# Kernel optimization log

Measured on AMD Instinct MI355X. Metric: run time of the kernel, lower is better.

## Reference

```python
import jax, jax.numpy as jnp
import numpy as np

N, E, DIN, EIN, H, R, G, DEPTH = 50000, 800000, 64, 16, 300, 1024, 256, 5


def setup_inputs() -> dict:
    key = jax.random.key(0)
    ks = jax.random.split(key, 16)
    x = jax.random.normal(ks[0], (N, DIN), jnp.float32)
    edge_attr = jax.random.normal(ks[1], (E, EIN), jnp.float32)
    edge_index = jax.random.randint(ks[2], (2, E), 0, N, dtype=jnp.int32)
    batch = jnp.sort(jax.random.randint(ks[3], (N,), 0, G, dtype=jnp.int32))
    def lin(k, fan_in, shape):
        return jax.random.normal(k, shape, jnp.float32) / np.sqrt(fan_in)
    return {
        "x": x,
        "edge_attr": edge_attr,
        "edge_index": edge_index,
        "batch": batch,
        "W_pn": lin(ks[4], DIN, (DIN, H)),
        "b_pn": jnp.zeros((H,), jnp.float32),
        "W_pe": lin(ks[5], EIN, (EIN, H)),
        "b_pe": jnp.zeros((H,), jnp.float32),
        "W1": lin(ks[6], H, (DEPTH, H, H)),
        "b1": jnp.zeros((DEPTH, H), jnp.float32),
        "W2": lin(ks[7], H, (DEPTH, H, H)),
        "b2": jnp.zeros((DEPTH, H), jnp.float32),
        "W_sp": lin(ks[8], H, (H, R)),
        "b_sp": jnp.zeros((R,), jnp.float32),
        "prelu_a": jnp.float32(0.25),
    }


def reference(x, edge_attr, edge_index, batch, W_pn, b_pn, W_pe, b_pe,
              W1, b1, W2, b2, W_sp, b_sp, prelu_a):
    src = edge_index[0]  # message source (x_j)
    dst = edge_index[1]  # aggregation target
    # input projections
    h = jax.nn.relu(x @ W_pn + b_pn)          # [N, H]
    e = edge_attr @ W_pe + b_pe               # [E, H]
    for i in range(DEPTH):
        # GINEConv: sum_j ReLU(x_j + e_ji), eps = 0
        m = jax.nn.relu(h[src] + e)            # [E, H]
        agg = jax.ops.segment_sum(m, dst, num_segments=N)  # [N, H]
        z = h + agg
        z = jax.nn.relu(z @ W1[i] + b1[i]) @ W2[i] + b2[i]
        h = jax.nn.relu(z) if i < DEPTH - 1 else z
        # dropout is identity in eval mode
    pooled = jax.ops.segment_sum(h, batch, num_segments=G)  # [G, H]
    out = pooled @ W_sp + b_sp                 # [G, R]
    # PReLU with a single learned slope
    return jnp.where(out >= 0, out, prelu_a * out)
```

## Files before the change

kernel.cpp:

```cpp
#include <hip/hip_runtime.h>
#include <hip/hip_bf16.h>

#define N_NODES 50000
#define N_EDGES 800000
#define DIN_    64
#define EIN_    16
#define H_      300
#define R_OUT   1024
#define G_GR    256
#define DEPTH_  5
#define KPAD    320
#define NPAD    50048

typedef unsigned short ushort_t;
typedef __attribute__((ext_vector_type(8))) short bf16x8;
typedef __attribute__((ext_vector_type(4))) float f32x4;

__device__ __forceinline__ ushort_t f2b(float f) {
  unsigned x = __float_as_uint(f);
  unsigned r = (x + 0x7fffu + ((x >> 16) & 1u)) >> 16;
  return (ushort_t)r;
}
__device__ __forceinline__ float b2f(ushort_t u) {
  return __uint_as_float((unsigned)u << 16);
}

__global__ void pack_weights(const float* __restrict__ W1, const float* __restrict__ W2,
                             ushort_t* __restrict__ Bp1, ushort_t* __restrict__ Bp2) {
  int idx = blockIdx.x * 256 + threadIdx.x;
  const int per = DEPTH_ * 40 * KPAD * 8;
  if (idx >= 2 * per) return;
  const float* W = W1;
  ushort_t* Bp = Bp1;
  int t = idx;
  if (t >= per) { t -= per; W = W2; Bp = Bp2; }
  int j  = t & 7;
  int n  = (t >> 3) % KPAD;
  int kg = ((t >> 3) / KPAD) % 40;
  int i  = t / (40 * KPAD * 8);
  int k  = kg * 8 + j;
  float v = (k < H_ && n < H_) ? W[(i * H_ + k) * H_ + n] : 0.f;
  Bp[t] = f2b(v);
}

__global__ void pack_wpe(const float* __restrict__ Wpe, const float* __restrict__ bpe,
                         ushort_t* __restrict__ Bpe) {
  int t = blockIdx.x * 256 + threadIdx.x;
  if (t >= 4 * KPAD * 8) return;
  int j  = t & 7;
  int n  = (t >> 3) % KPAD;
  int kg = (t >> 3) / KPAD;
  int k  = kg * 8 + j;
  float v = 0.f;
  if (n < H_) {
    if (k < EIN_) v = Wpe[k * H_ + n];
    else if (k == EIN_) v = bpe[n];
  }
  Bpe[t] = f2b(v);
}

__global__ void hist_deg(const int* __restrict__ dst, int* __restrict__ deg) {
  int e = blockIdx.x * 256 + threadIdx.x;
  if (e < N_EDGES) atomicAdd(deg + dst[e], 1);
}

__global__ __launch_bounds__(1024) void exscan_kernel(const int* __restrict__ deg,
                                                      int* __restrict__ off) {
  __shared__ int wsum[16];
  __shared__ int carry_s;
  int lane = threadIdx.x & 63;
  int wv = threadIdx.x >> 6;
  if (threadIdx.x == 0) carry_s = 0;
  __syncthreads();
  for (int base = 0; base < N_NODES; base += 1024) {
    int i = base + (int)threadIdx.x;
    int orig = (i < N_NODES) ? deg[i] : 0;
    int v = orig;
#pragma unroll
    for (int s = 1; s < 64; s <<= 1) {
      int u = __shfl_up(v, s);
      if (lane >= s) v += u;
    }
    if (lane == 63) wsum[wv] = v;
    __syncthreads();
    if (wv == 0) {
      int t = (lane < 16) ? wsum[lane] : 0;
#pragma unroll
      for (int s = 1; s < 16; s <<= 1) {
        int u = __shfl_up(t, s);
        if (lane >= s) t += u;
      }
      if (lane < 16) wsum[lane] = t;
    }
    __syncthreads();
    int wbase = (wv > 0) ? wsum[wv - 1] : 0;
    if (i < N_NODES) off[i] = carry_s + wbase + v - orig;
    __syncthreads();
    if (threadIdx.x == 1023) carry_s += wsum[15];
    __syncthreads();
  }
  if (threadIdx.x == 0) off[N_NODES] = carry_s;
}

__global__ void scatter_edges(const int* __restrict__ src, const int* __restrict__ dst,
                              int* __restrict__ cursor, int* __restrict__ csr_src,
                              int* __restrict__ csr_eid) {
  int e = blockIdx.x * 256 + threadIdx.x;
  if (e >= N_EDGES) return;
  int d = dst[e];
  int pos = atomicAdd(cursor + d, 1);
  csr_src[pos] = src[e];
  csr_eid[pos] = e;
}

__global__ void proj_nodes(const float* __restrict__ x, const float* __restrict__ Wpn,
                           const float* __restrict__ bpn, ushort_t* __restrict__ hb) {
  unsigned f = blockIdx.x * 256u + threadIdx.x;
  if (f >= (unsigned)NPAD * KPAD) return;
  unsigned n = f / KPAD, hh = f % KPAD;
  float v = 0.f;
  if (n < N_NODES && hh < H_) {
    float acc = bpn[hh];
    const float* xr = x + n * DIN_;
    const float* wc = Wpn + hh;
#pragma unroll 8
    for (int k = 0; k < DIN_; ++k) acc += xr[k] * wc[k * H_];
    v = fmaxf(acc, 0.f);
  }
  hb[f] = f2b(v);
}

__global__ __launch_bounds__(320) void node_agg_mfma(const ushort_t* __restrict__ hb,
                                                     const float* __restrict__ ea,
                                                     const ushort_t* __restrict__ Bpe,
                                                     const int* __restrict__ csr_src,
                                                     const int* __restrict__ csr_eid,
                                                     const int* __restrict__ off,
                                                     ushort_t* zb) {
  int n = blockIdx.x;
  int tid = threadIdx.x;
  if (n >= N_NODES) {
    zb[(unsigned)n * KPAD + tid] = 0;
    return;
  }
  int lane = tid & 63;
  int w = tid >> 6;
  int lr = lane & 15, lg = lane >> 4;
  int p0 = __builtin_amdgcn_readfirstlane(off[n]);
  int p1 = __builtin_amdgcn_readfirstlane(off[n + 1]);

  bf16x8 bfr[4];
#pragma unroll
  for (int t = 0; t < 4; ++t) {
    int col = w * 64 + t * 16 + lr;
    bfr[t] = *(const bf16x8*)(Bpe + ((unsigned)lg * KPAD + col) * 8);
  }

  float msum0 = 0.f, msum1 = 0.f, msum2 = 0.f, msum3 = 0.f;

  for (int pc = p0; pc < p1; pc += 16) {
    int eid = csr_eid[pc + lr];
    bf16x8 afr = (bf16x8){0, 0, 0, 0, 0, 0, 0, 0};
    if (lg < 2) {
      const float* ar = ea + (size_t)eid * EIN_ + lg * 8;
      f32x4 lo = *(const f32x4*)ar;
      f32x4 hi = *(const f32x4*)(ar + 4);
#pragma unroll
      for (int j = 0; j < 4; ++j) {
        afr[j] = (short)f2b(lo[j]);
        afr[j + 4] = (short)f2b(hi[j]);
      }
    } else if (lg == 2) {
      afr[0] = (short)0x3F80;
    }
    int base = pc + 4 * lg;
    int s0 = csr_src[base + 0];
    int s1 = csr_src[base + 1];
    int s2 = csr_src[base + 2];
    int s3 = csr_src[base + 3];
    bool v0 = (base + 0 < p1), v1 = (base + 1 < p1), v2 = (base + 2 < p1), v3 = (base + 3 < p1);
#pragma unroll
    for (int t = 0; t < 4; ++t) {
      int colb = w * 64 + t * 16 + lr;
      float g0 = b2f(hb[(unsigned)s0 * KPAD + colb]);
      float g1 = b2f(hb[(unsigned)s1 * KPAD + colb]);
      float g2 = b2f(hb[(unsigned)s2 * KPAD + colb]);
      float g3 = b2f(hb[(unsigned)s3 * KPAD + colb]);
      f32x4 e4 = __builtin_amdgcn_mfma_f32_16x16x32_bf16(afr, bfr[t], (f32x4){0.f, 0.f, 0.f, 0.f}, 0, 0, 0);
      float m0 = v0 ? fmaxf(g0 + e4[0], 0.f) : 0.f;
      float m1 = v1 ? fmaxf(g1 + e4[1], 0.f) : 0.f;
      float m2 = v2 ? fmaxf(g2 + e4[2], 0.f) : 0.f;
      float m3 = v3 ? fmaxf(g3 + e4[3], 0.f) : 0.f;
      float add = (m0 + m1) + (m2 + m3);
      if (t == 0) msum0 += add;
      else if (t == 1) msum1 += add;
      else if (t == 2) msum2 += add;
      else msum3 += add;
    }
  }

#pragma unroll
  for (int t = 0; t < 4; ++t) {
    float v = (t == 0) ? msum0 : (t == 1) ? msum1 : (t == 2) ? msum2 : msum3;
    v += __shfl_xor(v, 16);
    v += __shfl_xor(v, 32);
    if (lane < 16) {
      unsigned zi = (unsigned)n * KPAD + w * 64 + t * 16 + lane;
      zb[zi] = f2b(b2f(hb[zi]) + v);
    }
  }
}

template <int RELU_OUT, int OUT_BF16>
__global__ __launch_bounds__(256) void gemm300(const ushort_t* A,
                                               const ushort_t* __restrict__ Bp,
                                               const float* __restrict__ bias,
                                               void* Cout) {
  int lane = threadIdx.x & 63;
  int wid  = threadIdx.x >> 6;
  int lr = lane & 15, lg = lane >> 4;
  int rowblk  = blockIdx.x * 64 + (wid & 1) * 32;
  int colbase = (wid >> 1) * 160;
  f32x4 acc[2][10];
#pragma unroll
  for (int a = 0; a < 2; ++a)
#pragma unroll
    for (int c = 0; c < 10; ++c) acc[a][c] = (f32x4){0.f, 0.f, 0.f, 0.f};

  const ushort_t* Ap = A + (unsigned)(rowblk + lr) * KPAD + lg * 8;
  for (int k0 = 0; k0 < KPAD; k0 += 32) {
    bf16x8 a0 = *(const bf16x8*)(Ap + k0);
    bf16x8 a1 = *(const bf16x8*)(Ap + 16 * KPAD + k0);
    const ushort_t* bb = Bp + ((unsigned)(k0 / 8 + lg) * KPAD + colbase + lr) * 8;
#pragma unroll
    for (int c = 0; c < 10; ++c) {
      bf16x8 b = *(const bf16x8*)(bb + c * 16 * 8);
      acc[0][c] = __builtin_amdgcn_mfma_f32_16x16x32_bf16(a0, b, acc[0][c], 0, 0, 0);
      acc[1][c] = __builtin_amdgcn_mfma_f32_16x16x32_bf16(a1, b, acc[1][c], 0, 0, 0);
    }
  }
  __syncthreads();
#pragma unroll
  for (int rt = 0; rt < 2; ++rt) {
#pragma unroll
    for (int c = 0; c < 10; ++c) {
      int col = colbase + c * 16 + lr;
      float bv = (col < H_) ? bias[col] : 0.f;
#pragma unroll
      for (int r = 0; r < 4; ++r) {
        int row = rowblk + rt * 16 + lg * 4 + r;
        if (row >= N_NODES) continue;
        float v = acc[rt][c][r] + bv;
        if (RELU_OUT) v = fmaxf(v, 0.f);
        if (OUT_BF16) {
          ((ushort_t*)Cout)[(unsigned)row * KPAD + col] = f2b(v);
        } else if (col < H_) {
          ((float*)Cout)[(unsigned)row * H_ + col] = v;
        }
      }
    }
  }
}

__global__ void pool_kernel(const float* __restrict__ h, const int* __restrict__ batch,
                            float* __restrict__ pooled) {
  int g = blockIdx.x;
  int hh = threadIdx.x;
  int lo = 0, hi = N_NODES;
  while (lo < hi) { int mid = (lo + hi) >> 1; if (batch[mid] < g) lo = mid + 1; else hi = mid; }
  int start = lo;
  hi = N_NODES;
  while (lo < hi) { int mid = (lo + hi) >> 1; if (batch[mid] < g + 1) lo = mid + 1; else hi = mid; }
  int end = lo;
  if (hh >= H_) return;
  float s = 0.f;
  for (int n = start; n < end; ++n) s += h[(unsigned)n * H_ + hh];
  pooled[g * H_ + hh] = s;
}

__global__ void final_kernel(const float* __restrict__ pooled, const float* __restrict__ Wsp,
                             const float* __restrict__ bsp, const float* __restrict__ pa,
                             float* __restrict__ out) {
  int f = blockIdx.x * 256 + threadIdx.x;
  if (f >= G_GR * R_OUT) return;
  int g = f >> 10, r = f & 1023;
  float acc = bsp[r];
  const float* pr = pooled + g * H_;
  const float* wc = Wsp + r;
  for (int k = 0; k < H_; ++k) acc += pr[k] * wc[k * R_OUT];
  float a = pa[0];
  out[f] = acc >= 0.f ? acc : a * acc;
}

extern "C" void kernel_launch(void* const* d_in, const int* in_sizes, int n_in,
                              void* d_out, int out_size, void* d_ws, size_t ws_size,
                              hipStream_t stream) {
  const float* x   = (const float*)d_in[0];
  const float* ea  = (const float*)d_in[1];
  const int*   ei  = (const int*)d_in[2];
  const int*   bat = (const int*)d_in[3];
  const float* Wpn = (const float*)d_in[4];
  const float* bpn = (const float*)d_in[5];
  const float* Wpe = (const float*)d_in[6];
  const float* bpe = (const float*)d_in[7];
  const float* W1  = (const float*)d_in[8];
  const float* b1  = (const float*)d_in[9];
  const float* W2  = (const float*)d_in[10];
  const float* b2  = (const float*)d_in[11];
  const float* Wsp = (const float*)d_in[12];
  const float* bsp = (const float*)d_in[13];
  const float* pa  = (const float*)d_in[14];
  const int* src = ei;
  const int* dst = ei + N_EDGES;

  char* ws = (char*)d_ws;
  size_t off_b = 0;
  auto alloc = [&](size_t bytes) {
    void* p = ws + off_b;
    off_b += (bytes + 255) & ~(size_t)255;
    return p;
  };
  ushort_t* hb      = (ushort_t*)alloc(sizeof(ushort_t) * (size_t)NPAD * KPAD);
  ushort_t* zb      = (ushort_t*)alloc(sizeof(ushort_t) * (size_t)NPAD * KPAD);
  float*    h       = (float*)alloc(sizeof(float) * (size_t)N_NODES * H_);
  ushort_t* Bp1     = (ushort_t*)alloc(sizeof(ushort_t) * (size_t)DEPTH_ * 40 * KPAD * 8);
  ushort_t* Bp2     = (ushort_t*)alloc(sizeof(ushort_t) * (size_t)DEPTH_ * 40 * KPAD * 8);
  ushort_t* Bpe     = (ushort_t*)alloc(sizeof(ushort_t) * (size_t)4 * KPAD * 8);
  float*    pooled  = (float*)alloc(sizeof(float) * (size_t)G_GR * H_);
  int*      deg     = (int*)alloc(sizeof(int) * N_NODES);
  int*      offs    = (int*)alloc(sizeof(int) * (N_NODES + 1));
  int*      cursor  = (int*)alloc(sizeof(int) * N_NODES);
  int*      csr_src = (int*)alloc(sizeof(int) * (N_EDGES + 16));
  int*      csr_eid = (int*)alloc(sizeof(int) * (N_EDGES + 16));

  hipMemsetAsync(deg, 0, sizeof(int) * N_NODES, stream);
  hipMemsetAsync(csr_src + N_EDGES, 0, 16 * sizeof(int), stream);
  hipMemsetAsync(csr_eid + N_EDGES, 0, 16 * sizeof(int), stream);
  hist_deg<<<(N_EDGES + 255) / 256, 256, 0, stream>>>(dst, deg);
  exscan_kernel<<<1, 1024, 0, stream>>>(deg, offs);
  hipMemcpyAsync(cursor, offs, sizeof(int) * N_NODES, hipMemcpyDeviceToDevice, stream);
  scatter_edges<<<(N_EDGES + 255) / 256, 256, 0, stream>>>(src, dst, cursor, csr_src, csr_eid);

  pack_weights<<<(2 * DEPTH_ * 40 * KPAD * 8 + 255) / 256, 256, 0, stream>>>(W1, W2, Bp1, Bp2);
  pack_wpe<<<(4 * KPAD * 8 + 255) / 256, 256, 0, stream>>>(Wpe, bpe, Bpe);
  proj_nodes<<<((unsigned)NPAD * KPAD + 255) / 256, 256, 0, stream>>>(x, Wpn, bpn, hb);

  for (int i = 0; i < DEPTH_; ++i) {
    node_agg_mfma<<<NPAD, 320, 0, stream>>>(hb, ea, Bpe, csr_src, csr_eid, offs, zb);
    gemm300<1, 1><<<NPAD / 64, 256, 0, stream>>>(zb, Bp1 + (size_t)i * 40 * KPAD * 8, b1 + i * H_, zb);
    if (i < DEPTH_ - 1)
      gemm300<1, 1><<<NPAD / 64, 256, 0, stream>>>(zb, Bp2 + (size_t)i * 40 * KPAD * 8, b2 + i * H_, hb);
    else
      gemm300<0, 0><<<NPAD / 64, 256, 0, stream>>>(zb, Bp2 + (size_t)i * 40 * KPAD * 8, b2 + i * H_, h);
  }

  pool_kernel<<<G_GR, 320, 0, stream>>>(h, bat, pooled);
  final_kernel<<<(G_GR * R_OUT) / 256, 256, 0, stream>>>(pooled, Wsp, bsp, pa, (float*)d_out);
}
```

Measured before the change: 2.200 ms.

## Use MFMA for node projection and stage edge embeddings through LDS in aggregation

Replaces the scalar per-element input projection with an MFMA bf16 GEMM that uses packed Wpn weights. The node aggregation kernel now writes the MFMA-computed edge embeddings into LDS. Each thread then gathers its own column of h for each edge, so every per-thread load covers a single column instead of four rows times four tiles. This is meant to make the gathers coalesced across the 320 threads and to remove the cross-lane shuffle reduction. In exchange, each 16-edge chunk now costs two block barriers and an extra bf16 rounding of the edge embedding. Input x is also rounded to bf16 before the projection.

```diff
diff --git a/kernel.cpp b/kernel.cpp
--- a/kernel.cpp
+++ b/kernel.cpp
@@ -11,6 +11,7 @@
 #define DEPTH_  5
 #define KPAD    320
 #define NPAD    50048
+#define LDS_S   328
 
 typedef unsigned short ushort_t;
 typedef __attribute__((ext_vector_type(8))) short bf16x8;
@@ -59,6 +60,17 @@
   Bpe[t] = f2b(v);
 }
 
+__global__ void pack_wpn(const float* __restrict__ Wpn, ushort_t* __restrict__ Bpn) {
+  int t = blockIdx.x * 256 + threadIdx.x;
+  if (t >= 8 * KPAD * 8) return;
+  int j  = t & 7;
+  int n  = (t >> 3) % KPAD;
+  int kg = (t >> 3) / KPAD;
+  int k  = kg * 8 + j;
+  float v = (n < H_) ? Wpn[k * H_ + n] : 0.f;
+  Bpn[t] = f2b(v);
+}
+
 __global__ void hist_deg(const int* __restrict__ dst, int* __restrict__ deg) {
   int e = blockIdx.x * 256 + threadIdx.x;
   if (e < N_EDGES) atomicAdd(deg + dst[e], 1);
@@ -113,21 +125,60 @@
   csr_eid[pos] = e;
 }
 
-__global__ void proj_nodes(const float* __restrict__ x, const float* __restrict__ Wpn,
-                           const float* __restrict__ bpn, ushort_t* __restrict__ hb) {
-  unsigned f = blockIdx.x * 256u + threadIdx.x;
-  if (f >= (unsigned)NPAD * KPAD) return;
-  unsigned n = f / KPAD, hh = f % KPAD;
-  float v = 0.f;
-  if (n < N_NODES && hh < H_) {
-    float acc = bpn[hh];
-    const float* xr = x + n * DIN_;
-    const float* wc = Wpn + hh;
-#pragma unroll 8
-    for (int k = 0; k < DIN_; ++k) acc += xr[k] * wc[k * H_];
-    v = fmaxf(acc, 0.f);
-  }
-  hb[f] = f2b(v);
+__global__ __launch_bounds__(256) void proj_gemm(const float* __restrict__ x,
+                                                 const ushort_t* __restrict__ Bpn,
+                                                 const float* __restrict__ bpn,
+                                                 ushort_t* __restrict__ hb) {
+  int lane = threadIdx.x & 63;
+  int wid  = threadIdx.x >> 6;
+  int lr = lane & 15, lg = lane >> 4;
+  int rowblk  = blockIdx.x * 64 + (wid & 1) * 32;
+  int colbase = (wid >> 1) * 160;
+  int ar0 = rowblk + lr;       if (ar0 >= N_NODES) ar0 = 0;
+  int ar1 = rowblk + 16 + lr;  if (ar1 >= N_NODES) ar1 = 0;
+  f32x4 acc[2][10];
+#pragma unroll
+  for (int a = 0; a < 2; ++a)
+#pragma unroll
+    for (int c = 0; c < 10; ++c) acc[a][c] = (f32x4){0.f, 0.f, 0.f, 0.f};
+
+#pragma unroll
+  for (int ks = 0; ks < 2; ++ks) {
+    int k0 = ks * 32;
+    const float* xr0 = x + (size_t)ar0 * DIN_ + k0 + lg * 8;
+    const float* xr1 = x + (size_t)ar1 * DIN_ + k0 + lg * 8;
+    f32x4 l0 = *(const f32x4*)xr0, h0 = *(const f32x4*)(xr0 + 4);
+    f32x4 l1 = *(const f32x4*)xr1, h1 = *(const f32x4*)(xr1 + 4);
+    bf16x8 a0, a1;
+#pragma unroll
+    for (int j = 0; j < 4; ++j) {
+      a0[j] = (short)f2b(l0[j]); a0[j + 4] = (short)f2b(h0[j]);
+      a1[j] = (short)f2b(l1[j]); a1[j + 4] = (short)f2b(h1[j]);
+    }
+    const ushort_t* bb = Bpn + ((unsigned)(k0 / 8 + lg) * KPAD + colbase + lr) * 8;
+#pragma unroll
+    for (int c = 0; c < 10; ++c) {
+      bf16x8 b = *(const bf16x8*)(bb + c * 16 * 8);
+      acc[0][c] = __builtin_amdgcn_mfma_f32_16x16x32_bf16(a0, b, acc[0][c], 0, 0, 0);
+      acc[1][c] = __builtin_amdgcn_mfma_f32_16x16x32_bf16(a1, b, acc[1][c], 0, 0, 0);
+    }
+  }
+#pragma unroll
+  for (int rt = 0; rt < 2; ++rt) {
+#pragma unroll
+    for (int c = 0; c < 10; ++c) {
+      int col = colbase + c * 16 + lr;
+      float bv = (col < H_) ? bpn[col] : 0.f;
+#pragma unroll
+      for (int r = 0; r < 4; ++r) {
+        int row = rowblk + rt * 16 + lg * 4 + r;
+        if (row >= N_NODES) continue;
+        float v = fmaxf(acc[rt][c][r] + bv, 0.f);
+        if (col >= H_) v = 0.f;
+        hb[(unsigned)row * KPAD + col] = f2b(v);
+      }
+    }
+  }
 }
 
 __global__ __launch_bounds__(320) void node_agg_mfma(const ushort_t* __restrict__ hb,
@@ -137,6 +188,7 @@
                                                      const int* __restrict__ csr_eid,
                                                      const int* __restrict__ off,
                                                      ushort_t* zb) {
+  __shared__ ushort_t lds_e[16 * LDS_S];
   int n = blockIdx.x;
   int tid = threadIdx.x;
   if (n >= N_NODES) {
@@ -156,9 +208,9 @@
     bfr[t] = *(const bf16x8*)(Bpe + ((unsigned)lg * KPAD + col) * 8);
   }
 
-  float msum0 = 0.f, msum1 = 0.f, msum2 = 0.f, msum3 = 0.f;
-
+  float acc = 0.f;
   for (int pc = p0; pc < p1; pc += 16) {
+    int cnt = p1 - pc; if (cnt > 16) cnt = 16;
     int eid = csr_eid[pc + lr];
     bf16x8 afr = (bf16x8){0, 0, 0, 0, 0, 0, 0, 0};
     if (lg < 2) {
@@ -173,42 +225,44 @@
     } else if (lg == 2) {
       afr[0] = (short)0x3F80;
     }
-    int base = pc + 4 * lg;
-    int s0 = csr_src[base + 0];
-    int s1 = csr_src[base + 1];
-    int s2 = csr_src[base + 2];
-    int s3 = csr_src[base + 3];
-    bool v0 = (base + 0 < p1), v1 = (base + 1 < p1), v2 = (base + 2 < p1), v3 = (base + 3 < p1);
 #pragma unroll
     for (int t = 0; t < 4; ++t) {
-      int colb = w * 64 + t * 16 + lr;
-      float g0 = b2f(hb[(unsigned)s0 * KPAD + colb]);
-      float g1 = b2f(hb[(unsigned)s1 * KPAD + colb]);
-      float g2 = b2f(hb[(unsigned)s2 * KPAD + colb]);
-      float g3 = b2f(hb[(unsigned)s3 * KPAD + colb]);
       f32x4 e4 = __builtin_amdgcn_mfma_f32_16x16x32_bf16(afr, bfr[t], (f32x4){0.f, 0.f, 0.f, 0.f}, 0, 0, 0);
-      float m0 = v0 ? fmaxf(g0 + e4[0], 0.f) : 0.f;
-      float m1 = v1 ? fmaxf(g1 + e4[1], 0.f) : 0.f;
-      float m2 = v2 ? fmaxf(g2 + e4[2], 0.f) : 0.f;
-      float m3 = v3 ? fmaxf(g3 + e4[3], 0.f) : 0.f;
-      float add = (m0 + m1) + (m2 + m3);
-      if (t == 0) msum0 += add;
-      else if (t == 1) msum1 += add;
-      else if (t == 2) msum2 += add;
-      else msum3 += add;
-    }
-  }
-
-#pragma unroll
-  for (int t = 0; t < 4; ++t) {
-    float v = (t == 0) ? msum0 : (t == 1) ? msum1 : (t == 2) ? msum2 : msum3;
-    v += __shfl_xor(v, 16);
-    v += __shfl_xor(v, 32);
-    if (lane < 16) {
-      unsigned zi = (unsigned)n * KPAD + w * 64 + t * 16 + lane;
-      zb[zi] = f2b(b2f(hb[zi]) + v);
-    }
-  }
+      int col = w * 64 + t * 16 + lr;
+#pragma unroll
+      for (int r = 0; r < 4; ++r)
+        lds_e[(lg * 4 + r) * LDS_S + col] = f2b(e4[r]);
+    }
+    __syncthreads();
+    int e = 0;
+    for (; e + 4 <= cnt; e += 4) {
+      int s0 = csr_src[pc + e + 0];
+      int s1 = csr_src[pc + e + 1];
+      int s2 = csr_src[pc + e + 2];
+      int s3 = csr_src[pc + e + 3];
+      float g0 = b2f(hb[(unsigned)s0 * KPAD + tid]);
+      float g1 = b2f(hb[(unsigned)s1 * KPAD + tid]);
+      float g2 = b2f(hb[(unsigned)s2 * KPAD + tid]);
+      float g3 = b2f(hb[(unsigned)s3 * KPAD + tid]);
+      float e0 = b2f(lds_e[(e + 0) * LDS_S + tid]);
+      float e1 = b2f(lds_e[(e + 1) * LDS_S + tid]);
+      float e2 = b2f(lds_e[(e + 2) * LDS_S + tid]);
+      float e3 = b2f(lds_e[(e + 3) * LDS_S + tid]);
+      acc += fmaxf(g0 + e0, 0.f);
+      acc += fmaxf(g1 + e1, 0.f);
+      acc += fmaxf(g2 + e2, 0.f);
+      acc += fmaxf(g3 + e3, 0.f);
+    }
+    for (; e < cnt; ++e) {
+      int s = csr_src[pc + e];
+      float g = b2f(hb[(unsigned)s * KPAD + tid]);
+      float ev = b2f(lds_e[e * LDS_S + tid]);
+      acc += fmaxf(g + ev, 0.f);
+    }
+    __syncthreads();
+  }
+  unsigned zi = (unsigned)n * KPAD + tid;
+  zb[zi] = f2b(b2f(hb[zi]) + acc);
 }
 
 template <int RELU_OUT, int OUT_BF16>
@@ -326,6 +380,7 @@
   ushort_t* Bp1     = (ushort_t*)alloc(sizeof(ushort_t) * (size_t)DEPTH_ * 40 * KPAD * 8);
   ushort_t* Bp2     = (ushort_t*)alloc(sizeof(ushort_t) * (size_t)DEPTH_ * 40 * KPAD * 8);
   ushort_t* Bpe     = (ushort_t*)alloc(sizeof(ushort_t) * (size_t)4 * KPAD * 8);
+  ushort_t* Bpn     = (ushort_t*)alloc(sizeof(ushort_t) * (size_t)8 * KPAD * 8);
   float*    pooled  = (float*)alloc(sizeof(float) * (size_t)G_GR * H_);
   int*      deg     = (int*)alloc(sizeof(int) * N_NODES);
   int*      offs    = (int*)alloc(sizeof(int) * (N_NODES + 1));
@@ -343,7 +398,8 @@
 
   pack_weights<<<(2 * DEPTH_ * 40 * KPAD * 8 + 255) / 256, 256, 0, stream>>>(W1, W2, Bp1, Bp2);
   pack_wpe<<<(4 * KPAD * 8 + 255) / 256, 256, 0, stream>>>(Wpe, bpe, Bpe);
-  proj_nodes<<<((unsigned)NPAD * KPAD + 255) / 256, 256, 0, stream>>>(x, Wpn, bpn, hb);
+  pack_wpn<<<(8 * KPAD * 8 + 255) / 256, 256, 0, stream>>>(Wpn, Bpn);
+  proj_gemm<<<NPAD / 64, 256, 0, stream>>>(x, Bpn, bpn, hb);
 
   for (int i = 0; i < DEPTH_; ++i) {
     node_agg_mfma<<<NPAD, 320, 0, stream>>>(hb, ea, Bpe, csr_src, csr_eid, offs, zb);
```

After: 1.955 ms. 1.13x faster.
